# Kernel optimization log

Measured on AMD Instinct MI355X. Metric: run time of the kernel, lower is better.

The kernel has to match this reference:

```python
import jax, jax.numpy as jnp
import numpy as np

HEADS = 24
KV_HEADS = 6
HEAD_DIM = 64


def _partial_rope(x, cos, sin):
    # x: [B, H, S, head_dim]; cos/sin: [S, rot_dim]; rotate first rot_dim dims
    rot_dim = cos.shape[-1]
    x_rot, x_pass = x[..., :rot_dim], x[..., rot_dim:]
    half = rot_dim // 2
    # use_real_unbind_dim=-2: reshape (..., 2, half) then unbind -> first/second half
    x_real, x_imag = x_rot[..., :half], x_rot[..., half:]
    x_rotated = jnp.concatenate([-x_imag, x_real], axis=-1)
    out = x_rot * cos[None, None] + x_rotated * sin[None, None]
    return jnp.concatenate([out, x_pass], axis=-1)


def setup_inputs() -> dict:
    key = jax.random.key(0)
    ks = jax.random.split(key, 8)
    B, S, D = 2, 2048, 1536
    kv_dim = KV_HEADS * HEAD_DIM
    rot_dim = 32
    hidden_states = jax.random.normal(ks[0], (B, S, D), dtype=jnp.float32)
    # realistic rotary cos/sin from inv-freq angles
    pos = jnp.arange(S, dtype=jnp.float32)
    inv_freq = 1.0 / (10000.0 ** (jnp.arange(0, rot_dim, 2, dtype=jnp.float32) / rot_dim))
    ang = pos[:, None] * inv_freq[None, :]  # [S, rot_dim//2]
    ang = jnp.concatenate([ang, ang], axis=-1)  # [S, rot_dim]
    cos, sin = jnp.cos(ang), jnp.sin(ang)
    Wq = jax.random.normal(ks[1], (D, D), dtype=jnp.float32) * 0.02
    Wk = jax.random.normal(ks[2], (D, kv_dim), dtype=jnp.float32) * 0.02
    Wv = jax.random.normal(ks[3], (D, kv_dim), dtype=jnp.float32) * 0.02
    Wo = jax.random.normal(ks[4], (D, D), dtype=jnp.float32) * 0.02
    bo = jnp.zeros((D,), dtype=jnp.float32)
    return {"hidden_states": hidden_states, "cos": cos, "sin": sin,
            "Wq": Wq, "Wk": Wk, "Wv": Wv, "Wo": Wo, "bo": bo}


def reference(hidden_states, cos, sin, Wq, Wk, Wv, Wo, bo):
    B, S, D = hidden_states.shape
    residual = hidden_states
    q = hidden_states @ Wq  # [B,S,D]
    k = hidden_states @ Wk  # [B,S,kv_dim]
    v = hidden_states @ Wv
    q = q.reshape(B, S, HEADS, HEAD_DIM).transpose(0, 2, 1, 3)       # [B,H,S,d]
    k = k.reshape(B, S, KV_HEADS, HEAD_DIM).transpose(0, 2, 1, 3)    # [B,Hkv,S,d]
    v = v.reshape(B, S, KV_HEADS, HEAD_DIM).transpose(0, 2, 1, 3)
    rep = HEADS // KV_HEADS
    k = jnp.repeat(k, rep, axis=1)  # GQA repeat_interleave -> [B,H,S,d]
    v = jnp.repeat(v, rep, axis=1)
    # partial RoPE on query and key (self-attention)
    q = _partial_rope(q, cos, sin)
    k = _partial_rope(k, cos, sin)
    scale = 1.0 / jnp.sqrt(jnp.float32(HEAD_DIM))
    scores = jnp.einsum('bhqd,bhkd->bhqk', q, k) * scale
    probs = jax.nn.softmax(scores, axis=-1)
    out = jnp.einsum('bhqk,bhkd->bhqd', probs, v)
    out = out.transpose(0, 2, 1, 3).reshape(B, S, D)
    out = out @ Wo + bo
    return out + residual
```

## Files before the change

### kernel.cpp

```cpp
#include <hip/hip_runtime.h>

#define HEADS 24
#define KVH   6
#define HD    64
#define BB    2
#define SS    2048
#define DD    1536
#define KVD   384
#define QKD   1920
#define MM    4096

typedef unsigned short ushort_t;
typedef __attribute__((ext_vector_type(8))) short short8;
typedef __attribute__((ext_vector_type(4))) short short4v;
typedef __attribute__((ext_vector_type(4))) float f32x4;

__device__ __forceinline__ ushort_t f2bf(float f) {
    union { float f; unsigned u; } v; v.f = f;
    return (ushort_t)((v.u + 0x8000u) >> 16);
}
__device__ __forceinline__ unsigned pk2(float a, float b) {
    union { float f; unsigned u; } x, y; x.f = a; y.f = b;
    return ((x.u + 0x8000u) >> 16) | (((y.u + 0x8000u) >> 16) << 16);
}
__device__ __forceinline__ unsigned pk2t(float a, float b) {
    union { float f; unsigned u; } x, y; x.f = a; y.f = b;
    return (x.u >> 16) | (y.u & 0xFFFF0000u);
}
__device__ __forceinline__ float fexp2(float s) {
    float t = fmaf(s, 8388608.0f, 1065055420.0f);
    union { int i; float f; } v; v.i = (int)t;
    return v.f;
}
__device__ __forceinline__ short8 lds_frag8(const ushort_t* p) {
    short4v lo = *(const short4v*)p;
    short4v hi = *(const short4v*)(p + 4);
    return __builtin_shufflevector(lo, hi, 0, 1, 2, 3, 4, 5, 6, 7);
}
__device__ __forceinline__ void glds16(const void* g, void* l) {
    __builtin_amdgcn_global_load_lds(
        (const __attribute__((address_space(1))) void*)g,
        (__attribute__((address_space(3))) void*)l, 16, 0, 0);
}

__device__ __forceinline__ void tconv_body(const float* __restrict__ in,
                                           ushort_t* __restrict__ out,
                                           int R, int C, int cb, int rb)
{
    __shared__ ushort_t tile[32][33];
    const int tx = threadIdx.x & 31, ty = threadIdx.x >> 5;
    const int c0 = cb * 32, r0 = rb * 32;
#pragma unroll
    for (int i = 0; i < 4; ++i)
        tile[ty + i * 8][tx] = f2bf(in[(size_t)(r0 + ty + i * 8) * C + c0 + tx]);
    __syncthreads();
#pragma unroll
    for (int i = 0; i < 4; ++i)
        out[(size_t)(c0 + ty + i * 8) * R + r0 + tx] = tile[tx][ty + i * 8];
}

#define NCVT (MM * DD / 4 / 256)
__global__ __launch_bounds__(256) void k_prep(const float* __restrict__ HS,
                                              const float* __restrict__ Wq,
                                              const float* __restrict__ Wk,
                                              const float* __restrict__ Wv,
                                              const float* __restrict__ Wo,
                                              ushort_t* __restrict__ Xbf,
                                              ushort_t* __restrict__ Wqt,
                                              ushort_t* __restrict__ Wkt,
                                              ushort_t* __restrict__ Wvt,
                                              ushort_t* __restrict__ Wot)
{
    int bid = blockIdx.x;
    if (bid < NCVT) {
        int i = bid * 256 + threadIdx.x;
        float4 v = ((const float4*)HS)[i];
        uint2 o = { pk2(v.x, v.y), pk2(v.z, v.w) };
        ((uint2*)Xbf)[i] = o;
        return;
    }
    bid -= NCVT;
    if (bid < 2304) { tconv_body(Wq, Wqt, DD, DD,  bid % 48, bid / 48); return; }
    bid -= 2304;
    if (bid < 576)  { tconv_body(Wk, Wkt, DD, KVD, bid % 12, bid / 12); return; }
    bid -= 576;
    if (bid < 576)  { tconv_body(Wv, Wvt, DD, KVD, bid % 12, bid / 12); return; }
    bid -= 576;
    tconv_body(Wo, Wot, DD, DD, bid % 48, bid / 48);
}

__global__ __launch_bounds__(256) void k_proj(const ushort_t* __restrict__ Xbf,
                                              const ushort_t* __restrict__ Wqt,
                                              const ushort_t* __restrict__ Wkt,
                                              const ushort_t* __restrict__ Wvt,
                                              const float* __restrict__ cosb,
                                              const float* __restrict__ sinb,
                                              ushort_t* __restrict__ QKVb,
                                              ushort_t* __restrict__ VT)
{
    __shared__ ushort_t As[128][32];
    __shared__ ushort_t Bs[128][32];
    const int t = threadIdx.x, lane = t & 63, wave = t >> 6;
    const int n16 = lane & 15, quad = lane >> 4;
    const int wr = wave >> 1, wc = wave & 1;
    const int srow = lane >> 2;
    const int scol = (lane & 3) * 8;

    if (blockIdx.x < 480) {
        const int nt = blockIdx.x % 15;
        const int n0 = nt * 128;
        const int m0 = (blockIdx.x / 15) * 128;
        const ushort_t* Bt; int nl, isq;
        if (nt < 12) { Bt = Wqt; nl = n0;      isq = 1; }
        else         { Bt = Wkt; nl = n0 - DD; isq = 0; }

        const size_t aoff0 = (size_t)(m0 + wave * 16 + srow) * DD + scol;
        const size_t aoff1 = (size_t)(m0 + (wave + 4) * 16 + srow) * DD + scol;
        const size_t boff0 = (size_t)(nl + wave * 16 + srow) * DD + scol;
        const size_t boff1 = (size_t)(nl + (wave + 4) * 16 + srow) * DD + scol;
        ushort_t* lA0 = &As[wave * 16][0];
        ushort_t* lA1 = &As[(wave + 4) * 16][0];
        ushort_t* lB0 = &Bs[wave * 16][0];
        ushort_t* lB1 = &Bs[(wave + 4) * 16][0];

        f32x4 acc[4][4] = {};
        for (int k0 = 0; k0 < DD; k0 += 32) {
            __syncthreads();
            glds16(Xbf + aoff0 + k0, lA0);
            glds16(Xbf + aoff1 + k0, lA1);
            glds16(Bt  + boff0 + k0, lB0);
            glds16(Bt  + boff1 + k0, lB1);
            __syncthreads();
            short8 af[4], bf8[4];
#pragma unroll
            for (int i = 0; i < 4; ++i) af[i]  = *(const short8*)&As[wr * 64 + i * 16 + n16][quad * 8];
#pragma unroll
            for (int j = 0; j < 4; ++j) bf8[j] = *(const short8*)&Bs[wc * 64 + j * 16 + n16][quad * 8];
#pragma unroll
            for (int i = 0; i < 4; ++i)
#pragma unroll
                for (int j = 0; j < 4; ++j)
                    acc[i][j] = __builtin_amdgcn_mfma_f32_16x16x32_bf16(af[i], bf8[j], acc[i][j], 0, 0, 0);
        }

        const float QSC = 0.18033688011112042f;
#pragma unroll
        for (int i = 0; i < 4; ++i) {
#pragma unroll
            for (int r = 0; r < 4; ++r) {
                const int row = m0 + wr * 64 + i * 16 + quad * 4 + r;
                ushort_t* outp = QKVb + (size_t)row * QKD + n0 + wc * 64 + n16;
                float v0 = acc[i][0][r], v1 = acc[i][1][r];
                float v2 = acc[i][2][r], v3 = acc[i][3][r];
                {
                    const int s = row & (SS - 1);
                    float c0 = cosb[s * 32 + n16],      s0 = sinb[s * 32 + n16];
                    float c1 = cosb[s * 32 + 16 + n16], s1 = sinb[s * 32 + 16 + n16];
                    float nr = v0 * c0 - v1 * s0;
                    float ni = v1 * c1 + v0 * s1;
                    v0 = nr; v1 = ni;
                }
                if (isq) { v0 *= QSC; v1 *= QSC; v2 *= QSC; v3 *= QSC; }
                outp[0]  = f2bf(v0);
                outp[16] = f2bf(v1);
                outp[32] = f2bf(v2);
                outp[48] = f2bf(v3);
            }
        }
    } else {
        const int vb = blockIdx.x - 480;
        const int n0 = (vb & 31) * 128;
        const int m0 = (vb >> 5) * 64;

        const size_t aoff  = (size_t)(m0 + wave * 16 + srow) * DD + scol;
        const size_t boff0 = (size_t)(n0 + wave * 32 + srow) * DD + scol;
        const size_t boff1 = boff0 + (size_t)16 * DD;
        ushort_t* lA  = &As[wave * 16][0];
        ushort_t* lB0 = &Bs[wave * 32][0];
        ushort_t* lB1 = &Bs[wave * 32 + 16][0];

        f32x4 acc[2][4] = {};
        for (int k0 = 0; k0 < DD; k0 += 32) {
            __syncthreads();
            glds16(Wvt + aoff  + k0, lA);
            glds16(Xbf + boff0 + k0, lB0);
            glds16(Xbf + boff1 + k0, lB1);
            __syncthreads();
            short8 af[2], bf8[4];
#pragma unroll
            for (int i = 0; i < 2; ++i) af[i]  = *(const short8*)&As[wr * 32 + i * 16 + n16][quad * 8];
#pragma unroll
            for (int j = 0; j < 4; ++j) bf8[j] = *(const short8*)&Bs[wc * 64 + j * 16 + n16][quad * 8];
#pragma unroll
            for (int i = 0; i < 2; ++i)
#pragma unroll
                for (int j = 0; j < 4; ++j)
                    acc[i][j] = __builtin_amdgcn_mfma_f32_16x16x32_bf16(af[i], bf8[j], acc[i][j], 0, 0, 0);
        }

        const int b = n0 >> 11;
#pragma unroll
        for (int i = 0; i < 2; ++i)
#pragma unroll
            for (int r = 0; r < 4; ++r) {
                const int c = m0 + wr * 32 + i * 16 + quad * 4 + r;
                ushort_t* op = VT + ((size_t)b * KVD + c) * SS +
                               (n0 & (SS - 1)) + wc * 64 + 4 * n16;
                uint2 o = { pk2(acc[i][0][r], acc[i][1][r]),
                            pk2(acc[i][2][r], acc[i][3][r]) };
                *(uint2*)op = o;
            }
    }
}

__global__ __launch_bounds__(256) void k_attn(const ushort_t* __restrict__ QKVb,
                                              const ushort_t* __restrict__ VT,
                                              ushort_t* __restrict__ AOb)
{
    __shared__ __align__(16) ushort_t Ks[64][76];
    __shared__ __align__(16) ushort_t Vs[64][76];
    __shared__ __align__(16) ushort_t Ps[128][76];

    const int t    = threadIdx.x;
    const int wave = t >> 6;
    const int quad = (t >> 4) & 3;
    const int n16  = t & 15;
    const int q0   = blockIdx.x * 128;
    const int h    = blockIdx.y;
    const int b    = blockIdx.z;
    const int kh   = h >> 2;

    const int sr = t >> 2;
    const int sc = (t & 3) * 8;
    const int vc = (t & 3) * 16;

    short8 qf[2][2];
#pragma unroll
    for (int m = 0; m < 2; ++m)
#pragma unroll
        for (int kc = 0; kc < 2; ++kc)
            qf[m][kc] = *(const short8*)(QKVb +
                (size_t)(b * SS + q0 + wave * 32 + m * 16 + n16) * QKD +
                h * HD + kc * 32 + quad * 8);

    float l_p[2][4] = {};
    f32x4 acc_o[2][4] = {};

    const ushort_t* Kbase = QKVb + (size_t)(b * SS) * QKD + DD + kh * HD;
    const ushort_t* Vbase = VT + ((size_t)b * KVD + kh * 64) * SS;

    for (int kt = 0; kt < SS / 64; ++kt) {
        const int k0 = kt * 64;
        __syncthreads();
        {
            const ushort_t* Kg = Kbase + (size_t)(k0 + sr) * QKD + sc;
            uint4 kv0 = *(const uint4*)(Kg);
            uint4 kv1 = *(const uint4*)(Kg + 32);
            *(uint2*)&Ks[sr][sc]      = make_uint2(kv0.x, kv0.y);
            *(uint2*)&Ks[sr][sc + 4]  = make_uint2(kv0.z, kv0.w);
            *(uint2*)&Ks[sr][sc + 32] = make_uint2(kv1.x, kv1.y);
            *(uint2*)&Ks[sr][sc + 36] = make_uint2(kv1.z, kv1.w);
            const ushort_t* Vg = Vbase + (size_t)sr * SS + k0 + vc;
            uint4 vv0 = *(const uint4*)(Vg);
            uint4 vv1 = *(const uint4*)(Vg + 8);
            *(uint2*)&Vs[sr][vc]      = make_uint2(vv0.x, vv0.y);
            *(uint2*)&Vs[sr][vc + 4]  = make_uint2(vv0.z, vv0.w);
            *(uint2*)&Vs[sr][vc + 8]  = make_uint2(vv1.x, vv1.y);
            *(uint2*)&Vs[sr][vc + 12] = make_uint2(vv1.z, vv1.w);
        }
        __syncthreads();

        f32x4 s_acc[2][4] = {};
#pragma unroll
        for (int kc = 0; kc < 2; ++kc) {
            short8 bf[4];
#pragma unroll
            for (int jj = 0; jj < 4; ++jj)
                bf[jj] = lds_frag8(&Ks[jj * 16 + n16][kc * 32 + quad * 8]);
#pragma unroll
            for (int m = 0; m < 2; ++m)
#pragma unroll
                for (int jj = 0; jj < 4; ++jj)
                    s_acc[m][jj] = __builtin_amdgcn_mfma_f32_16x16x32_bf16(
                        qf[m][kc], bf[jj], s_acc[m][jj], 0, 0, 0);
        }

#pragma unroll
        for (int m = 0; m < 2; ++m)
#pragma unroll
            for (int r = 0; r < 4; ++r) {
                float p0 = fexp2(s_acc[m][0][r]);
                float p1 = fexp2(s_acc[m][1][r]);
                float p2 = fexp2(s_acc[m][2][r]);
                float p3 = fexp2(s_acc[m][3][r]);
                uint2 o = { pk2t(p0, p1), pk2t(p2, p3) };
                *(uint2*)&Ps[wave * 32 + m * 16 + quad * 4 + r][4 * n16] = o;
                l_p[m][r] += (p0 + p1) + (p2 + p3);
            }

#pragma unroll
        for (int kc = 0; kc < 2; ++kc) {
            short8 vb[4];
#pragma unroll
            for (int dd = 0; dd < 4; ++dd)
                vb[dd] = lds_frag8(&Vs[dd * 16 + n16][kc * 32 + quad * 8]);
#pragma unroll
            for (int m = 0; m < 2; ++m) {
                short8 pa = lds_frag8(&Ps[wave * 32 + m * 16 + n16][kc * 32 + quad * 8]);
#pragma unroll
                for (int dd = 0; dd < 4; ++dd)
                    acc_o[m][dd] = __builtin_amdgcn_mfma_f32_16x16x32_bf16(
                        pa, vb[dd], acc_o[m][dd], 0, 0, 0);
            }
        }
    }

#pragma unroll
    for (int m = 0; m < 2; ++m) {
        float inv[4];
#pragma unroll
        for (int r = 0; r < 4; ++r) {
            float s = l_p[m][r];
#pragma unroll
            for (int msk = 1; msk < 16; msk <<= 1)
                s += __shfl_xor(s, msk);
            inv[r] = 1.0f / s;
        }
#pragma unroll
        for (int dd = 0; dd < 4; ++dd)
#pragma unroll
            for (int r = 0; r < 4; ++r) {
                int q = q0 + wave * 32 + m * 16 + quad * 4 + r;
                AOb[(size_t)(b * SS + q) * DD + h * HD + dd * 16 + n16] =
                    f2bf(acc_o[m][dd][r] * inv[r]);
            }
    }
}

__global__ __launch_bounds__(256) void k_out_mfma(const ushort_t* __restrict__ AOb,
                                                  const ushort_t* __restrict__ Wot,
                                                  const float* __restrict__ bo,
                                                  const float* __restrict__ HS,
                                                  float* __restrict__ out)
{
    __shared__ ushort_t As[64][32];
    __shared__ ushort_t Bs[128][32];
    const int t = threadIdx.x, lane = t & 63, wave = t >> 6;
    const int n16 = lane & 15, quad = lane >> 4;
    const int wr = wave >> 1, wc = wave & 1;
    const int n0 = blockIdx.x * 128;
    const int m0 = blockIdx.y * 64;

    const int srow = lane >> 2;
    const int scol = (lane & 3) * 8;
    const size_t aoff  = (size_t)(m0 + wave * 16 + srow) * DD + scol;
    const size_t boff0 = (size_t)(n0 + wave * 32 + srow) * DD + scol;
    const size_t boff1 = boff0 + (size_t)16 * DD;
    ushort_t* lA  = &As[wave * 16][0];
    ushort_t* lB0 = &Bs[wave * 32][0];
    ushort_t* lB1 = &Bs[wave * 32 + 16][0];

    f32x4 acc[2][4] = {};
    for (int k0 = 0; k0 < DD; k0 += 32) {
        __syncthreads();
        glds16(AOb + aoff  + k0, lA);
        glds16(Wot + boff0 + k0, lB0);
        glds16(Wot + boff1 + k0, lB1);
        __syncthreads();
        short8 af[2], bf8[4];
#pragma unroll
        for (int i = 0; i < 2; ++i) af[i]  = *(const short8*)&As[wr * 32 + i * 16 + n16][quad * 8];
#pragma unroll
        for (int j = 0; j < 4; ++j) bf8[j] = *(const short8*)&Bs[wc * 64 + j * 16 + n16][quad * 8];
#pragma unroll
        for (int i = 0; i < 2; ++i)
#pragma unroll
            for (int j = 0; j < 4; ++j)
                acc[i][j] = __builtin_amdgcn_mfma_f32_16x16x32_bf16(af[i], bf8[j], acc[i][j], 0, 0, 0);
    }

    const int colb = n0 + wc * 64 + n16;
    float bo4[4];
#pragma unroll
    for (int j = 0; j < 4; ++j) bo4[j] = bo[colb + j * 16];
#pragma unroll
    for (int i = 0; i < 2; ++i) {
#pragma unroll
        for (int r = 0; r < 4; ++r) {
            const int row = m0 + wr * 32 + i * 16 + quad * 4 + r;
            float* op = out + (size_t)row * DD + colb;
            const float* hp = HS + (size_t)row * DD + colb;
#pragma unroll
            for (int j = 0; j < 4; ++j)
                op[j * 16] = acc[i][j][r] + bo4[j] + hp[j * 16];
        }
    }
}

extern "C" void kernel_launch(void* const* d_in, const int* in_sizes, int n_in,
                              void* d_out, int out_size, void* d_ws, size_t ws_size,
                              hipStream_t stream)
{
    const float* HS   = (const float*)d_in[0];
    const float* cosb = (const float*)d_in[1];
    const float* sinb = (const float*)d_in[2];
    const float* Wq   = (const float*)d_in[3];
    const float* Wk   = (const float*)d_in[4];
    const float* Wv   = (const float*)d_in[5];
    const float* Wo   = (const float*)d_in[6];
    const float* bo   = (const float*)d_in[7];
    float* out = (float*)d_out;

    ushort_t* Xbf  = (ushort_t*)d_ws;
    ushort_t* QKVb = Xbf  + (size_t)MM * DD;
    ushort_t* AOb  = QKVb + (size_t)MM * QKD;
    ushort_t* Wqt  = AOb  + (size_t)MM * DD;
    ushort_t* Wkt  = Wqt  + (size_t)DD * DD;
    ushort_t* Wvt  = Wkt  + (size_t)KVD * DD;
    ushort_t* Wot  = Wvt  + (size_t)KVD * DD;
    ushort_t* VT   = Wot  + (size_t)DD * DD;

    const int nprep = NCVT + 2304 + 576 + 576 + 2304;
    k_prep    <<<dim3(nprep), 256, 0, stream>>>(HS, Wq, Wk, Wv, Wo,
                                                Xbf, Wqt, Wkt, Wvt, Wot);
    k_proj    <<<dim3(480 + 192), 256, 0, stream>>>(Xbf, Wqt, Wkt, Wvt,
                                                    cosb, sinb, QKVb, VT);
    k_attn    <<<dim3(SS / 128, HEADS, BB), 256, 0, stream>>>(QKVb, VT, AOb);
    k_out_mfma<<<dim3(DD / 128, MM / 64),   256, 0, stream>>>(AOb, Wot, bo, HS, out);
}
```

Before: 260.9 us.

## Compute transposed scores to keep P in registers, dropping LDS round-trip

The attention kernel now computes S^T by swapping the MFMA operands, so each lane holds the probabilities in the layout the PV MFMA needs as its B operand. P no longer goes through the shared-memory Ps tile, which removes LDS writes and reads and frees shared memory. To make this work, the V-transpose kernel writes V columns in a permuted order that matches the register packing. The output is then normalized with a simpler two-step shuffle and written with vectorized stores. The risk is that the permuted key ordering must line up exactly across kernels, or the results will be wrong.

```diff
diff --git a/kernel.cpp b/kernel.cpp
--- a/kernel.cpp
+++ b/kernel.cpp
@@ -199,16 +199,16 @@
         }
 
         const int b = n0 >> 11;
+        const int s0 = 8 * (n16 >> 2) + 2 * (n16 & 3);
 #pragma unroll
         for (int i = 0; i < 2; ++i)
 #pragma unroll
             for (int r = 0; r < 4; ++r) {
                 const int c = m0 + wr * 32 + i * 16 + quad * 4 + r;
                 ushort_t* op = VT + ((size_t)b * KVD + c) * SS +
-                               (n0 & (SS - 1)) + wc * 64 + 4 * n16;
-                uint2 o = { pk2(acc[i][0][r], acc[i][1][r]),
-                            pk2(acc[i][2][r], acc[i][3][r]) };
-                *(uint2*)op = o;
+                               (n0 & (SS - 1)) + wc * 64 + s0;
+                *(unsigned*)op        = pk2(acc[i][0][r], acc[i][1][r]);
+                *(unsigned*)(op + 32) = pk2(acc[i][2][r], acc[i][3][r]);
             }
     }
 }
@@ -219,7 +219,6 @@
 {
     __shared__ __align__(16) ushort_t Ks[64][76];
     __shared__ __align__(16) ushort_t Vs[64][76];
-    __shared__ __align__(16) ushort_t Ps[128][76];
 
     const int t    = threadIdx.x;
     const int wave = t >> 6;
@@ -243,7 +242,7 @@
                 (size_t)(b * SS + q0 + wave * 32 + m * 16 + n16) * QKD +
                 h * HD + kc * 32 + quad * 8);
 
-    float l_p[2][4] = {};
+    float l_p[2] = {};
     f32x4 acc_o[2][4] = {};
 
     const ushort_t* Kbase = QKVb + (size_t)(b * SS) * QKD + DD + kh * HD;
@@ -270,7 +269,7 @@
         }
         __syncthreads();
 
-        f32x4 s_acc[2][4] = {};
+        f32x4 sT[2][4] = {};
 #pragma unroll
         for (int kc = 0; kc < 2; ++kc) {
             short8 bf[4];
@@ -281,22 +280,25 @@
             for (int m = 0; m < 2; ++m)
 #pragma unroll
                 for (int jj = 0; jj < 4; ++jj)
-                    s_acc[m][jj] = __builtin_amdgcn_mfma_f32_16x16x32_bf16(
-                        qf[m][kc], bf[jj], s_acc[m][jj], 0, 0, 0);
-        }
-
-#pragma unroll
-        for (int m = 0; m < 2; ++m)
-#pragma unroll
-            for (int r = 0; r < 4; ++r) {
-                float p0 = fexp2(s_acc[m][0][r]);
-                float p1 = fexp2(s_acc[m][1][r]);
-                float p2 = fexp2(s_acc[m][2][r]);
-                float p3 = fexp2(s_acc[m][3][r]);
-                uint2 o = { pk2t(p0, p1), pk2t(p2, p3) };
-                *(uint2*)&Ps[wave * 32 + m * 16 + quad * 4 + r][4 * n16] = o;
-                l_p[m][r] += (p0 + p1) + (p2 + p3);
+                    sT[m][jj] = __builtin_amdgcn_mfma_f32_16x16x32_bf16(
+                        bf[jj], qf[m][kc], sT[m][jj], 0, 0, 0);
+        }
+
+        union PB { unsigned w[4]; short8 v; };
+        PB pb[2][2];
+#pragma unroll
+        for (int m = 0; m < 2; ++m) {
+#pragma unroll
+            for (int w = 0; w < 4; ++w) {
+                float p0 = fexp2(sT[m][0][w]);
+                float p1 = fexp2(sT[m][1][w]);
+                float p2 = fexp2(sT[m][2][w]);
+                float p3 = fexp2(sT[m][3][w]);
+                pb[m][0].w[w] = pk2t(p0, p1);
+                pb[m][1].w[w] = pk2t(p2, p3);
+                l_p[m] += (p0 + p1) + (p2 + p3);
             }
+        }
 
 #pragma unroll
         for (int kc = 0; kc < 2; ++kc) {
@@ -305,35 +307,28 @@
             for (int dd = 0; dd < 4; ++dd)
                 vb[dd] = lds_frag8(&Vs[dd * 16 + n16][kc * 32 + quad * 8]);
 #pragma unroll
-            for (int m = 0; m < 2; ++m) {
-                short8 pa = lds_frag8(&Ps[wave * 32 + m * 16 + n16][kc * 32 + quad * 8]);
+            for (int m = 0; m < 2; ++m)
 #pragma unroll
                 for (int dd = 0; dd < 4; ++dd)
                     acc_o[m][dd] = __builtin_amdgcn_mfma_f32_16x16x32_bf16(
-                        pa, vb[dd], acc_o[m][dd], 0, 0, 0);
-            }
+                        vb[dd], pb[m][kc].v, acc_o[m][dd], 0, 0, 0);
         }
     }
 
 #pragma unroll
     for (int m = 0; m < 2; ++m) {
-        float inv[4];
-#pragma unroll
-        for (int r = 0; r < 4; ++r) {
-            float s = l_p[m][r];
-#pragma unroll
-            for (int msk = 1; msk < 16; msk <<= 1)
-                s += __shfl_xor(s, msk);
-            inv[r] = 1.0f / s;
-        }
-#pragma unroll
-        for (int dd = 0; dd < 4; ++dd)
-#pragma unroll
-            for (int r = 0; r < 4; ++r) {
-                int q = q0 + wave * 32 + m * 16 + quad * 4 + r;
-                AOb[(size_t)(b * SS + q) * DD + h * HD + dd * 16 + n16] =
-                    f2bf(acc_o[m][dd][r] * inv[r]);
-            }
+        float s = l_p[m];
+        s += __shfl_xor(s, 16);
+        s += __shfl_xor(s, 32);
+        const float inv = 1.0f / s;
+        const int q = q0 + wave * 32 + m * 16 + n16;
+        ushort_t* op = AOb + (size_t)(b * SS + q) * DD + h * HD + quad * 4;
+#pragma unroll
+        for (int dd = 0; dd < 4; ++dd) {
+            uint2 o = { pk2(acc_o[m][dd][0] * inv, acc_o[m][dd][1] * inv),
+                        pk2(acc_o[m][dd][2] * inv, acc_o[m][dd][3] * inv) };
+            *(uint2*)(op + dd * 16) = o;
+        }
     }
 }
 
```

Measured after the change: 259.0 us. About the same (-0.7%).
